# Kernel tuning notes

Hardware: AMD Instinct MI355X
Metric: run time of the kernel (lower is better)

Reference implementation:

```python
import jax, jax.numpy as jnp
import numpy as np

B, T, D = 8, 16384, 128


def setup_inputs() -> dict:
    key = jax.random.key(0)
    ks = jax.random.split(key, 14)
    sc = lambda fan_in: 1.0 / np.sqrt(fan_in)
    x = jax.random.normal(ks[0], (B, T, D), jnp.float32)
    return {
        "x": x,
        # BindingField (scale 0): bind_key / bind_query Linear(D, D//2)
        "Wk": jax.random.normal(ks[1], (D, D // 2), jnp.float32) * sc(D),
        "bk": jnp.zeros((D // 2,), jnp.float32),
        "Wq": jax.random.normal(ks[2], (D, D // 2), jnp.float32) * sc(D),
        "bq": jnp.zeros((D // 2,), jnp.float32),
        # aggregator (scale 0): Linear(D,D) -> LayerNorm(D) -> ReLU -> Linear(D,D)
        "Wa1": jax.random.normal(ks[3], (D, D), jnp.float32) * sc(D),
        "ba1": jnp.zeros((D,), jnp.float32),
        "ln_g": jnp.ones((D,), jnp.float32),
        "ln_b": jnp.zeros((D,), jnp.float32),
        "Wa2": jax.random.normal(ks[4], (D, D), jnp.float32) * sc(D),
        "ba2": jnp.zeros((D,), jnp.float32),
        # downward_influence (scale 0): Linear(D,D)
        "Wd": jax.random.normal(ks[5], (D, D), jnp.float32) * sc(D),
        "bd": jnp.zeros((D,), jnp.float32),
    }


def reference(x, Wk, bk, Wq, bq, Wa1, ba1, ln_g, ln_b, Wa2, ba2, Wd, bd):
    Bn, Tn, Dn = x.shape
    BIND_THRESHOLD = 0.5
    LN_EPS = 1e-5

    # ---- BindingField: binding strength between adjacent tokens ----
    keys = x[:, :-1] @ Wk + bk                       # [B, T-1, D/2]
    queries = x[:, 1:] @ Wq + bq                     # [B, T-1, D/2]
    strength = jax.nn.sigmoid((keys * queries).sum(-1) / float(np.sqrt(Dn // 2)))
    bind = strength > BIND_THRESHOLD                 # [B, T-1]

    # chunk_starts: token 0 always starts; token t starts iff NOT bound to t-1
    chunk_starts = jnp.concatenate([jnp.ones((Bn, 1), bool), ~bind], axis=1)
    seg = jnp.cumsum(chunk_starts.astype(jnp.int32), axis=1) - 1  # [B, T] chunk id per token

    # ---- aggregate_chunks: ragged mean-pool via segment_sum (pad to T chunk slots) ----
    seg_flat = (seg + jnp.arange(Bn, dtype=jnp.int32)[:, None] * Tn).reshape(-1)
    sums = jax.ops.segment_sum(x.reshape(-1, Dn), seg_flat, num_segments=Bn * Tn)
    counts = jax.ops.segment_sum(jnp.ones((Bn * Tn,), x.dtype), seg_flat,
                                 num_segments=Bn * Tn)
    chunk_mean = (sums / jnp.maximum(counts, 1.0)[:, None]).reshape(Bn, Tn, Dn)

    # aggregator MLP: Linear -> LayerNorm -> ReLU -> Linear
    h = chunk_mean @ Wa1 + ba1
    mu = h.mean(-1, keepdims=True)
    var = ((h - mu) ** 2).mean(-1, keepdims=True)    # biased var, as torch LayerNorm
    h = (h - mu) * jax.lax.rsqrt(var + LN_EPS) * ln_g + ln_b
    agg = jax.nn.relu(h) @ Wa2 + ba2                 # [B, T(chunk slots), D]

    # ---- apply_downward_influence: broadcast chunk signal back to its tokens ----
    infl = agg @ Wd + bd                             # [B, T(chunks), D]
    gathered = jnp.take_along_axis(infl, seg[..., None].astype(jnp.int32), axis=1)
    gate = jax.nn.sigmoid(gathered)
    return x * gate + x
```

## Files before the change

### kernel.cpp

```cpp
#include <hip/hip_runtime.h>
#include <math.h>

#define BB 8
#define TT 16384
#define DD 128
#define DH 64
#define FCAP 32768
#define FMARGIN 0.05f

typedef _Float16 half8 __attribute__((ext_vector_type(8)));
typedef float f32x4 __attribute__((ext_vector_type(4)));

union H8 { half8 h; uint4 q; ushort us[8]; };

static __device__ __forceinline__ float4 ld4(const float* p) { return *(const float4*)p; }

static __device__ __forceinline__ uint pk2(float a, float b) {
    union { _Float16 f; ushort u; } A, B;
    A.f = (_Float16)a; B.f = (_Float16)b;
    return (uint)A.u | ((uint)B.u << 16);
}

static __device__ __forceinline__ void split8h(const float4 v0, const float4 v1,
                                               half8* xh, half8* xl)
{
    float f[8] = {v0.x, v0.y, v0.z, v0.w, v1.x, v1.y, v1.z, v1.w};
    half8 h, l;
    #pragma unroll
    for (int j = 0; j < 8; ++j) {
        _Float16 hv = (_Float16)f[j];
        h[j] = hv;
        l[j] = (_Float16)(f[j] - (float)hv);
    }
    *xh = h; *xl = l;
}

__global__ __launch_bounds__(64) void k_wprep(
    const float* __restrict__ Wa1, const float* __restrict__ Wa2,
    const float* __restrict__ Wd, const float* __restrict__ Wk,
    const float* __restrict__ Wq, ushort* __restrict__ wfm,
    ushort* __restrict__ wfb, int* __restrict__ fcnt)
{
    const int l  = threadIdx.x;
    const int nt = blockIdx.x & 7;
    const int kb = blockIdx.x >> 3;
    const int ly = blockIdx.y;
    if (ly == 0 && blockIdx.x == 0 && l == 0) *fcnt = 0;
    const int n  = nt * 16 + (l & 15);
    const int k0 = kb * 32 + (l >> 4) * 8;
    H8 v;
    if (ly < 3) {
        const float* W = (ly == 0) ? Wa1 : (ly == 1) ? Wa2 : Wd;
        #pragma unroll
        for (int e = 0; e < 8; ++e) v.h[e] = (_Float16)W[(k0 + e) * DD + n];
        *(uint4*)(wfm + (size_t)(((ly * 8 + nt) * 4 + kb) * 64 + l) * 8) = v.q;
    } else {
        #pragma unroll
        for (int e = 0; e < 8; ++e) {
            float w = (n < 64) ? Wk[(k0 + e) * DH + n] : Wq[(k0 + e) * DH + n - 64];
            v.h[e] = (_Float16)w;
        }
        *(uint4*)(wfb + (size_t)((nt * 4 + kb) * 64 + l) * 8) = v.q;
    }
}

__global__ __launch_bounds__(256, 2) void k_bind(
    const float* __restrict__ x, const ushort* __restrict__ wfb,
    const float* __restrict__ bk, const float* __restrict__ bq,
    int* __restrict__ cstart, int* __restrict__ flist, int* __restrict__ fcnt)
{
    __shared__ uint4 Bs4[2048];
    __shared__ float bnd[4][64];
    const int b    = blockIdx.y;
    const int tb   = blockIdx.x * 64;
    const int tid  = threadIdx.x;
    const int wv   = tid >> 6;
    const int l    = tid & 63;
    const int lo16 = l & 15;
    const int g    = l >> 4;

    {
        const uint4* wsrc = (const uint4*)wfb;
        #pragma unroll
        for (int j = 0; j < 8; ++j) { int idx = tid + j * 256; Bs4[idx] = wsrc[idx]; }
    }

    const float* xrow = x + ((size_t)b * TT + tb + wv * 16 + lo16) * DD;
    half8 xh[4], xl[4];
    #pragma unroll
    for (int kb = 0; kb < 4; ++kb) {
        float4 v0 = ld4(xrow + kb * 32 + g * 8);
        float4 v1 = ld4(xrow + kb * 32 + g * 8 + 4);
        split8h(v0, v1, &xh[kb], &xl[kb]);
    }
    int r64 = tb + 64; if (r64 > TT - 1) r64 = TT - 1;
    const float* xq = x + ((size_t)b * TT + r64) * DD;
    half8 qh[4], ql[4];
    H8 z; z.q.x = z.q.y = z.q.z = z.q.w = 0u;
    #pragma unroll
    for (int kb = 0; kb < 4; ++kb) {
        qh[kb] = z.h; ql[kb] = z.h;
        if (lo16 == 0) {
            float4 v0 = ld4(xq + kb * 32 + g * 8);
            float4 v1 = ld4(xq + kb * 32 + g * 8 + 4);
            split8h(v0, v1, &qh[kb], &ql[kb]);
        }
    }

    f32x4 acc[8];
    #pragma unroll
    for (int nt = 0; nt < 8; ++nt) {
        int col = nt * 16 + lo16;
        float bias = (col < 64) ? bk[col] : bq[col - 64];
        acc[nt] = (f32x4){bias, bias, bias, bias};
    }
    f32x4 acc4;
    {
        float bias = bq[wv * 16 + lo16];
        acc4 = (f32x4){bias, bias, bias, bias};
    }

    __syncthreads();
    const ushort* Bs = (const ushort*)Bs4;
    const ushort* Bs_halo = Bs + (size_t)((4 + wv) * 4 * 64 + l) * 8;
    #pragma unroll
    for (int kb = 0; kb < 4; ++kb) {
        half8 bh[8];
        #pragma unroll
        for (int nt = 0; nt < 8; ++nt)
            bh[nt] = *(const half8*)(Bs + (size_t)((nt * 4 + kb) * 64 + l) * 8);
        #pragma unroll
        for (int nt = 0; nt < 8; ++nt) {
            acc[nt] = __builtin_amdgcn_mfma_f32_16x16x32_f16(xh[kb], bh[nt], acc[nt], 0, 0, 0);
            acc[nt] = __builtin_amdgcn_mfma_f32_16x16x32_f16(xl[kb], bh[nt], acc[nt], 0, 0, 0);
        }
        half8 bh4 = *(const half8*)(Bs_halo + (size_t)kb * 64 * 8);
        acc4 = __builtin_amdgcn_mfma_f32_16x16x32_f16(qh[kb], bh4, acc4, 0, 0, 0);
        acc4 = __builtin_amdgcn_mfma_f32_16x16x32_f16(ql[kb], bh4, acc4, 0, 0, 0);
    }

    if (l < 16) {
        if (wv > 0) {
            #pragma unroll
            for (int nt = 0; nt < 4; ++nt) bnd[wv - 1][nt * 16 + lo16] = acc[4 + nt][0];
        }
        bnd[3][wv * 16 + lo16] = acc4[0];
    }
    __syncthreads();

    float qn3[4];
    #pragma unroll
    for (int nt = 0; nt < 4; ++nt) qn3[nt] = __shfl_down(acc[4 + nt][0], 16);
    if (g == 3) {
        #pragma unroll
        for (int nt = 0; nt < 4; ++nt) qn3[nt] = bnd[wv][nt * 16 + lo16];
    }
    float s[4];
    #pragma unroll
    for (int i = 0; i < 3; ++i) {
        float t = 0.f;
        #pragma unroll
        for (int nt = 0; nt < 4; ++nt) t += acc[nt][i] * acc[4 + nt][i + 1];
        s[i] = t;
    }
    {
        float t = 0.f;
        #pragma unroll
        for (int nt = 0; nt < 4; ++nt) t += acc[nt][3] * qn3[nt];
        s[3] = t;
    }
    #pragma unroll
    for (int i = 0; i < 4; ++i) {
        #pragma unroll
        for (int m = 1; m < 16; m <<= 1) s[i] += __shfl_xor(s[i], m);
    }
    if (lo16 == 0) {
        #pragma unroll
        for (int i = 0; i < 4; ++i) {
            int t = tb + wv * 16 + g * 4 + i;
            if (t <= TT - 2) {
                cstart[b * TT + t + 1] = (s[i] > 0.f) ? 0 : 1;
                if (fabsf(s[i]) < FMARGIN) {
                    int pos = atomicAdd(fcnt, 1);
                    if (pos < FCAP) flist[pos] = b * TT + t;
                }
            }
        }
    }
    if (blockIdx.x == 0 && tid == 0) cstart[b * TT] = 1;
}

__global__ __launch_bounds__(256) void k_fixup(
    const float* __restrict__ x, const float* __restrict__ Wk, const float* __restrict__ bk,
    const float* __restrict__ Wq, const float* __restrict__ bq,
    const int* __restrict__ flist, const int* __restrict__ fcnt, int* __restrict__ cstart)
{
    const int n    = min(*fcnt, FCAP);
    const int wv   = (blockIdx.x * 256 + threadIdx.x) >> 6;
    const int lane = threadIdx.x & 63;
    const int nwv  = gridDim.x * 4;
    for (int i = wv; i < n; i += nwv) {
        int idx = flist[i];
        int b = idx >> 14;
        int t = idx & (TT - 1);
        const float* xt = x + ((size_t)b * TT + t) * DD;
        float K = bk[lane], Q = bq[lane];
        #pragma unroll 8
        for (int k = 0; k < DD; ++k) {
            K = fmaf(xt[k],      Wk[k * DH + lane], K);
            Q = fmaf(xt[DD + k], Wq[k * DH + lane], Q);
        }
        float p = K * Q;
        #pragma unroll
        for (int m = 1; m < 64; m <<= 1) p += __shfl_xor(p, m);
        if (lane == 0) cstart[b * TT + t + 1] = (p > 0.f) ? 0 : 1;
    }
}

__global__ __launch_bounds__(1024) void k_scan(const int* __restrict__ cstart,
    int* __restrict__ seg, int* __restrict__ cs, int* __restrict__ numC)
{
    __shared__ int wsum[16];
    const int b = blockIdx.x, tid = threadIdx.x;
    const int wv = tid >> 6, lane = tid & 63;
    const int base = b * TT + tid * 16;
    int v[16];
    #pragma unroll
    for (int i = 0; i < 4; ++i) {
        int4 q = *(const int4*)(cstart + base + i * 4);
        v[i * 4 + 0] = q.x; v[i * 4 + 1] = q.y; v[i * 4 + 2] = q.z; v[i * 4 + 3] = q.w;
    }
    int s[16]; int run = 0;
    #pragma unroll
    for (int i = 0; i < 16; ++i) { run += v[i]; s[i] = run; }
    int incl = run;
    #pragma unroll
    for (int off = 1; off < 64; off <<= 1) {
        int t = __shfl_up(incl, off);
        if (lane >= off) incl += t;
    }
    if (lane == 63) wsum[wv] = incl;
    __syncthreads();
    if (tid < 16) {
        int w = wsum[tid];
        #pragma unroll
        for (int off = 1; off < 16; off <<= 1) {
            int t = __shfl_up(w, off, 16);
            if (tid >= off) w += t;
        }
        wsum[tid] = w;
    }
    __syncthreads();
    const int excl = (wv ? wsum[wv - 1] : 0) + incl - run;
    #pragma unroll
    for (int i = 0; i < 16; ++i) {
        int sg = excl + s[i] - 1;
        seg[base + i] = sg;
        if (v[i]) cs[b * (TT + 1) + sg] = tid * 16 + i;
    }
    if (tid == 1023) {
        int tot = excl + run;
        numC[b] = tot;
        cs[b * (TT + 1) + tot] = TT;
    }
}

__device__ __forceinline__ void mlp_gemm(f32x4 acc[8], const uint4* Afr4,
    const ushort* Bs, int wv, int l)
{
    half8 af[4];
    #pragma unroll
    for (int kb = 0; kb < 4; ++kb)
        af[kb] = *(const half8*)((const char*)Afr4 + ((wv * 4 + kb) * 64 + l) * 16);
    #pragma unroll
    for (int kb = 0; kb < 4; ++kb) {
        half8 bh[8];
        #pragma unroll
        for (int nt = 0; nt < 8; ++nt)
            bh[nt] = *(const half8*)(Bs + (size_t)((nt * 4 + kb) * 64 + l) * 8);
        #pragma unroll
        for (int nt = 0; nt < 8; ++nt)
            acc[nt] = __builtin_amdgcn_mfma_f32_16x16x32_f16(af[kb], bh[nt], acc[nt], 0, 0, 0);
    }
}

__global__ __launch_bounds__(256, 2) void k_mlp(
    const float* __restrict__ x, const int* __restrict__ cs,
    const float* __restrict__ ba1, const float* __restrict__ ln_g, const float* __restrict__ ln_b,
    const float* __restrict__ ba2, const float* __restrict__ bd,
    const ushort* __restrict__ wfm, const int* __restrict__ numC, float* __restrict__ cm)
{
    __shared__ union {
        float Tok[64 * 132];
        struct { uint4 Afr[1024]; uint4 Bs[2048]; } fb;
    } sm;
    const int b  = blockIdx.y;
    const int nC = numC[b];
    const int c0 = blockIdx.x * 64;
    if (c0 >= nC) return;
    const int tid  = threadIdx.x;
    const int wv   = tid >> 6;
    const int l    = tid & 63;
    const int lo16 = l & 15;
    const int g    = l >> 4;
    const ushort* Bs = (const ushort*)sm.fb.Bs;
    const uint4* wsrc = (const uint4*)wfm;

    const int cbase = b * (TT + 1);
    const int T0 = cs[cbase + c0];
    const int cEnd = (c0 + 64 < nC) ? (c0 + 64) : nC;
    const int T1 = cs[cbase + cEnd];
    int t0r[8], t1r[8];
    #pragma unroll
    for (int ii = 0; ii < 8; ++ii) {
        int r = (tid + ii * 256) >> 5;
        int c = c0 + r;
        t0r[ii] = (c < nC) ? cs[cbase + c] : 0;
        t1r[ii] = (c < nC) ? cs[cbase + c + 1] : 0;
    }
    float4 vals[8];
    #pragma unroll
    for (int ii = 0; ii < 8; ++ii) vals[ii] = make_float4(0.f, 0.f, 0.f, 0.f);

    for (int tt = T0; tt < T1; tt += 64) {
        __syncthreads();
        const int tEnd = (tt + 64 < T1) ? (tt + 64) : T1;
        for (int j = tid; j < (tEnd - tt) * 32; j += 256) {
            int trow = j >> 5, c4 = (j & 31) * 4;
            *(float4*)&sm.Tok[trow * 132 + c4] =
                ld4(x + ((size_t)b * TT + tt + trow) * DD + c4);
        }
        __syncthreads();
        #pragma unroll
        for (int ii = 0; ii < 8; ++ii) {
            int c4 = ((tid + ii * 256) & 31) * 4;
            int lo = (t0r[ii] > tt)   ? t0r[ii] : tt;
            int hi = (t1r[ii] < tEnd) ? t1r[ii] : tEnd;
            for (int t = lo; t < hi; ++t) {
                const float* ap = &sm.Tok[(t - tt) * 132 + c4];
                vals[ii].x += ap[0]; vals[ii].y += ap[1];
                vals[ii].z += ap[2]; vals[ii].w += ap[3];
            }
        }
    }
    __syncthreads();

    #pragma unroll
    for (int ii = 0; ii < 8; ++ii) {
        int i = tid + ii * 256;
        int r = i >> 5, c4 = (i & 31) * 4;
        float4 sv = make_float4(0.f, 0.f, 0.f, 0.f);
        if (c0 + r < nC) {
            float inv = 1.f / (float)(t1r[ii] - t0r[ii]);
            sv.x = vals[ii].x * inv; sv.y = vals[ii].y * inv;
            sv.z = vals[ii].z * inv; sv.w = vals[ii].w * inv;
        }
        int frag = (r >> 4) * 4 + (c4 >> 5);
        int lanef = (r & 15) + (((c4 & 31) >> 3) * 16);
        uint2 pk = make_uint2(pk2(sv.x, sv.y), pk2(sv.z, sv.w));
        *(uint2*)((char*)sm.fb.Afr + frag * 1024 + lanef * 16 + (c4 & 7) * 2) = pk;
    }
    #pragma unroll
    for (int j = 0; j < 8; ++j) { int idx = tid + j * 256; sm.fb.Bs[idx] = wsrc[idx]; }
    __syncthreads();

    f32x4 acc[8];
    #pragma unroll
    for (int nt = 0; nt < 8; ++nt) {
        float bias = ba1[nt * 16 + lo16];
        acc[nt] = (f32x4){bias, bias, bias, bias};
    }
    mlp_gemm(acc, sm.fb.Afr, Bs, wv, l);

    float mu_[4], rs_[4];
    #pragma unroll
    for (int i = 0; i < 4; ++i) {
        float smv = 0.f;
        #pragma unroll
        for (int nt = 0; nt < 8; ++nt) smv += acc[nt][i];
        #pragma unroll
        for (int k = 1; k < 16; k <<= 1) smv += __shfl_xor(smv, k, 16);
        mu_[i] = smv * (1.f / 128.f);
        float vs = 0.f;
        #pragma unroll
        for (int nt = 0; nt < 8; ++nt) { float d = acc[nt][i] - mu_[i]; vs += d * d; }
        #pragma unroll
        for (int k = 1; k < 16; k <<= 1) vs += __shfl_xor(vs, k, 16);
        rs_[i] = rsqrtf(vs * (1.f / 128.f) + 1e-5f);
    }
    float gam[8], bet[8];
    #pragma unroll
    for (int nt = 0; nt < 8; ++nt) { gam[nt] = ln_g[nt * 16 + lo16]; bet[nt] = ln_b[nt * 16 + lo16]; }

    __syncthreads();
    #pragma unroll
    for (int nt = 0; nt < 8; ++nt) {
        int cw = nt * 16 + lo16;
        int frag = wv * 4 + (cw >> 5);
        int lnf  = (((cw & 31) >> 3) * 16);
        #pragma unroll
        for (int i = 0; i < 4; ++i) {
            float h = fmaf((acc[nt][i] - mu_[i]) * rs_[i], gam[nt], bet[nt]);
            union { _Float16 f; ushort u; } cv; cv.f = (_Float16)fmaxf(h, 0.f);
            *((ushort*)((char*)sm.fb.Afr + frag * 1024 + ((g * 4 + i) + lnf) * 16 + (cw & 7) * 2)) = cv.u;
        }
    }
    #pragma unroll
    for (int j = 0; j < 8; ++j) { int idx = tid + j * 256; sm.fb.Bs[idx] = wsrc[2048 + idx]; }
    __syncthreads();

    #pragma unroll
    for (int nt = 0; nt < 8; ++nt) {
        float bias = ba2[nt * 16 + lo16];
        acc[nt] = (f32x4){bias, bias, bias, bias};
    }
    mlp_gemm(acc, sm.fb.Afr, Bs, wv, l);
    __syncthreads();
    #pragma unroll
    for (int nt = 0; nt < 8; ++nt) {
        int cw = nt * 16 + lo16;
        int frag = wv * 4 + (cw >> 5);
        int lnf  = (((cw & 31) >> 3) * 16);
        #pragma unroll
        for (int i = 0; i < 4; ++i) {
            union { _Float16 f; ushort u; } cv; cv.f = (_Float16)acc[nt][i];
            *((ushort*)((char*)sm.fb.Afr + frag * 1024 + ((g * 4 + i) + lnf) * 16 + (cw & 7) * 2)) = cv.u;
        }
    }
    #pragma unroll
    for (int j = 0; j < 8; ++j) { int idx = tid + j * 256; sm.fb.Bs[idx] = wsrc[4096 + idx]; }
    __syncthreads();

    #pragma unroll
    for (int nt = 0; nt < 8; ++nt) {
        float bias = bd[nt * 16 + lo16];
        acc[nt] = (f32x4){bias, bias, bias, bias};
    }
    mlp_gemm(acc, sm.fb.Afr, Bs, wv, l);
    #pragma unroll
    for (int i = 0; i < 4; ++i) {
        int row = c0 + wv * 16 + g * 4 + i;
        if (row < nC) {
            float* dst = cm + ((size_t)b * TT + row) * DD + lo16;
            #pragma unroll
            for (int nt = 0; nt < 8; ++nt)
                dst[nt * 16] = 1.f / (1.f + __expf(-acc[nt][i]));
        }
    }
}

__global__ __launch_bounds__(256) void k_out(const float* __restrict__ x,
    const int* __restrict__ seg, const float* __restrict__ gate, float* __restrict__ out)
{
    const size_t idx = (size_t)blockIdx.x * 256 + threadIdx.x;
    const size_t tok = idx >> 5;
    const int d4 = (int)(idx & 31);
    const int b  = (int)(tok >> 14);
    const int sg = seg[tok];
    float4 gv = ld4(gate + (((size_t)b << 14) + sg) * DD + d4 * 4);
    float4 xv = ld4(x + tok * DD + (size_t)d4 * 4);
    float4 o;
    o.x = fmaf(xv.x, gv.x, xv.x);
    o.y = fmaf(xv.y, gv.y, xv.y);
    o.z = fmaf(xv.z, gv.z, xv.z);
    o.w = fmaf(xv.w, gv.w, xv.w);
    *(float4*)(out + idx * 4) = o;
}

extern "C" void kernel_launch(void* const* d_in, const int* in_sizes, int n_in,
                              void* d_out, int out_size, void* d_ws, size_t ws_size,
                              hipStream_t stream)
{
    (void)in_sizes; (void)n_in; (void)out_size; (void)ws_size;
    const float* x    = (const float*)d_in[0];
    const float* Wk   = (const float*)d_in[1];
    const float* bk   = (const float*)d_in[2];
    const float* Wq   = (const float*)d_in[3];
    const float* bq   = (const float*)d_in[4];
    const float* Wa1  = (const float*)d_in[5];
    const float* ba1  = (const float*)d_in[6];
    const float* ln_g = (const float*)d_in[7];
    const float* ln_b = (const float*)d_in[8];
    const float* Wa2  = (const float*)d_in[9];
    const float* ba2  = (const float*)d_in[10];
    const float* Wd   = (const float*)d_in[11];
    const float* bd   = (const float*)d_in[12];
    float* out = (float*)d_out;

    char* p = (char*)d_ws;
    float* cm    = (float*)p;   p += (size_t)BB * TT * DD * 4;
    int* seg     = (int*)p;     p += (size_t)BB * TT * 4;
    int* cs      = (int*)p;     p += (size_t)BB * (TT + 1) * 4;
    int* numC    = (int*)p;     p += 64;
    ushort* wfm  = (ushort*)p;  p += 3 * DD * DD * 2;
    ushort* wfb  = (ushort*)p;  p += DD * DD * 2;
    int* flist   = (int*)p;     p += (size_t)FCAP * 4;
    int* fcnt    = (int*)p;

    k_wprep<<<dim3(32, 4), 64, 0, stream>>>(Wa1, Wa2, Wd, Wk, Wq, wfm, wfb, fcnt);
    k_bind<<<dim3(256, BB), 256, 0, stream>>>(x, wfb, bk, bq, seg, flist, fcnt);
    k_fixup<<<dim3(256), 256, 0, stream>>>(x, Wk, bk, Wq, bq, flist, fcnt, seg);
    k_scan<<<dim3(BB), 1024, 0, stream>>>(seg, seg, cs, numC);
    k_mlp<<<dim3(TT / 64, BB), 256, 0, stream>>>(x, cs, ba1, ln_g, ln_b, ba2, bd, wfm, numC, cm);
    k_out<<<dim3(BB * TT * DD / (256 * 4)), 256, 0, stream>>>(x, seg, cm, out);
}
```

Measured before the change: 118.2 us.

## Fuse gated output into MLP kernel and prefetch weights through registers

Removes the separate output kernel and the chunk-gate buffer in global memory. Each MLP block now stages its 64 sigmoid gates (plus one) in shared memory and writes the outputs for all tokens its chunks cover, re-reading x for that token range. Weight tiles for the next GEMM are also prefetched into registers before the preceding shared-memory phase, which hides global load latency but adds register pressure at the 2-blocks-per-SM bound. Saves the gate write and read plus one kernel launch, but the output pass is now serialized inside each block after the three GEMMs.

```diff
diff --git a/kernel.cpp b/kernel.cpp
--- a/kernel.cpp
+++ b/kernel.cpp
@@ -285,10 +285,10 @@
 }
 
 __global__ __launch_bounds__(256, 2) void k_mlp(
-    const float* __restrict__ x, const int* __restrict__ cs,
+    const float* __restrict__ x, const int* __restrict__ cs, const int* __restrict__ seg,
     const float* __restrict__ ba1, const float* __restrict__ ln_g, const float* __restrict__ ln_b,
     const float* __restrict__ ba2, const float* __restrict__ bd,
-    const ushort* __restrict__ wfm, const int* __restrict__ numC, float* __restrict__ cm)
+    const ushort* __restrict__ wfm, const int* __restrict__ numC, float* __restrict__ out)
 {
     __shared__ union {
         float Tok[64 * 132];
@@ -306,6 +306,10 @@
     const ushort* Bs = (const ushort*)sm.fb.Bs;
     const uint4* wsrc = (const uint4*)wfm;
 
+    uint4 breg[8];
+    #pragma unroll
+    for (int j = 0; j < 8; ++j) breg[j] = wsrc[tid + j * 256];
+
     const int cbase = b * (TT + 1);
     const int T0 = cs[cbase + c0];
     const int cEnd = (c0 + 64 < nC) ? (c0 + 64) : nC;
@@ -346,6 +350,8 @@
     __syncthreads();
 
     #pragma unroll
+    for (int j = 0; j < 8; ++j) sm.fb.Bs[tid + j * 256] = breg[j];
+    #pragma unroll
     for (int ii = 0; ii < 8; ++ii) {
         int i = tid + ii * 256;
         int r = i >> 5, c4 = (i & 31) * 4;
@@ -361,7 +367,7 @@
         *(uint2*)((char*)sm.fb.Afr + frag * 1024 + lanef * 16 + (c4 & 7) * 2) = pk;
     }
     #pragma unroll
-    for (int j = 0; j < 8; ++j) { int idx = tid + j * 256; sm.fb.Bs[idx] = wsrc[idx]; }
+    for (int j = 0; j < 8; ++j) breg[j] = wsrc[2048 + tid + j * 256];
     __syncthreads();
 
     f32x4 acc[8];
@@ -406,7 +412,9 @@
         }
     }
     #pragma unroll
-    for (int j = 0; j < 8; ++j) { int idx = tid + j * 256; sm.fb.Bs[idx] = wsrc[2048 + idx]; }
+    for (int j = 0; j < 8; ++j) sm.fb.Bs[tid + j * 256] = breg[j];
+    #pragma unroll
+    for (int j = 0; j < 8; ++j) breg[j] = wsrc[4096 + tid + j * 256];
     __syncthreads();
 
     #pragma unroll
@@ -428,7 +436,7 @@
         }
     }
     #pragma unroll
-    for (int j = 0; j < 8; ++j) { int idx = tid + j * 256; sm.fb.Bs[idx] = wsrc[4096 + idx]; }
+    for (int j = 0; j < 8; ++j) sm.fb.Bs[tid + j * 256] = breg[j];
     __syncthreads();
 
     #pragma unroll
@@ -437,34 +445,29 @@
         acc[nt] = (f32x4){bias, bias, bias, bias};
     }
     mlp_gemm(acc, sm.fb.Afr, Bs, wv, l);
-    #pragma unroll
-    for (int i = 0; i < 4; ++i) {
-        int row = c0 + wv * 16 + g * 4 + i;
-        if (row < nC) {
-            float* dst = cm + ((size_t)b * TT + row) * DD + lo16;
-            #pragma unroll
-            for (int nt = 0; nt < 8; ++nt)
-                dst[nt * 16] = 1.f / (1.f + __expf(-acc[nt][i]));
-        }
-    }
-}
-
-__global__ __launch_bounds__(256) void k_out(const float* __restrict__ x,
-    const int* __restrict__ seg, const float* __restrict__ gate, float* __restrict__ out)
-{
-    const size_t idx = (size_t)blockIdx.x * 256 + threadIdx.x;
-    const size_t tok = idx >> 5;
-    const int d4 = (int)(idx & 31);
-    const int b  = (int)(tok >> 14);
-    const int sg = seg[tok];
-    float4 gv = ld4(gate + (((size_t)b << 14) + sg) * DD + d4 * 4);
-    float4 xv = ld4(x + tok * DD + (size_t)d4 * 4);
-    float4 o;
-    o.x = fmaf(xv.x, gv.x, xv.x);
-    o.y = fmaf(xv.y, gv.y, xv.y);
-    o.z = fmaf(xv.z, gv.z, xv.z);
-    o.w = fmaf(xv.w, gv.w, xv.w);
-    *(float4*)(out + idx * 4) = o;
+    __syncthreads();
+
+    #pragma unroll
+    for (int nt = 0; nt < 8; ++nt) {
+        #pragma unroll
+        for (int i = 0; i < 4; ++i) {
+            int row = wv * 16 + g * 4 + i;
+            sm.Tok[row * 132 + nt * 16 + lo16] = 1.f + 1.f / (1.f + __expf(-acc[nt][i]));
+        }
+    }
+    __syncthreads();
+
+    for (int j = tid; j < (T1 - T0) * 32; j += 256) {
+        int tok = T0 + (j >> 5);
+        int c4  = (j & 31) * 4;
+        int row = seg[b * TT + tok] - c0;
+        float4 xv = ld4(x + ((size_t)b * TT + tok) * DD + c4);
+        float4 gv = *(const float4*)&sm.Tok[row * 132 + c4];
+        float4 o;
+        o.x = xv.x * gv.x; o.y = xv.y * gv.y;
+        o.z = xv.z * gv.z; o.w = xv.w * gv.w;
+        *(float4*)(out + ((size_t)b * TT + tok) * DD + c4) = o;
+    }
 }
 
 extern "C" void kernel_launch(void* const* d_in, const int* in_sizes, int n_in,
@@ -488,7 +491,7 @@
     float* out = (float*)d_out;
 
     char* p = (char*)d_ws;
-    float* cm    = (float*)p;   p += (size_t)BB * TT * DD * 4;
+    p += (size_t)BB * TT * DD * 4;
     int* seg     = (int*)p;     p += (size_t)BB * TT * 4;
     int* cs      = (int*)p;     p += (size_t)BB * (TT + 1) * 4;
     int* numC    = (int*)p;     p += 64;
@@ -501,6 +504,5 @@
     k_bind<<<dim3(256, BB), 256, 0, stream>>>(x, wfb, bk, bq, seg, flist, fcnt);
     k_fixup<<<dim3(256), 256, 0, stream>>>(x, Wk, bk, Wq, bq, flist, fcnt, seg);
     k_scan<<<dim3(BB), 1024, 0, stream>>>(seg, seg, cs, numC);
-    k_mlp<<<dim3(TT / 64, BB), 256, 0, stream>>>(x, cs, ba1, ln_g, ln_b, ba2, bd, wfm, numC, cm);
-    k_out<<<dim3(BB * TT * DD / (256 * 4)), 256, 0, stream>>>(x, seg, cm, out);
-}
+    k_mlp<<<dim3(TT / 64, BB), 256, 0, stream>>>(x, cs, seg, ba1, ln_g, ln_b, ba2, bd, wfm, numC, out);
+}
```

After: 129.9 us. 1.1x slower.

## Halve MLP chunk tile, prefetch weights in registers, store gate as fp16

Applied to the files above, without the earlier changes.

The chunk-MLP kernel now handles 32 chunks per block instead of 64, so twice as many blocks share the ragged workload and only two of the four waves run the GEMMs. Weight fragments for the next layer are prefetched into registers while the current stage computes, which hides the global load latency behind the pooling and GEMM work. The gate tensor is written and read as fp16 instead of fp32, halving gate traffic between the MLP and output kernels. The cost is idle waves during the GEMMs and a small precision loss in the gate.

```diff
diff --git a/kernel.cpp b/kernel.cpp
--- a/kernel.cpp
+++ b/kernel.cpp
@@ -19,6 +19,12 @@
     union { _Float16 f; ushort u; } A, B;
     A.f = (_Float16)a; B.f = (_Float16)b;
     return (uint)A.u | ((uint)B.u << 16);
+}
+static __device__ __forceinline__ ushort f2h(float a) {
+    union { _Float16 f; ushort u; } A; A.f = (_Float16)a; return A.u;
+}
+static __device__ __forceinline__ float h2f(ushort u) {
+    union { ushort u; _Float16 f; } A; A.u = u; return (float)A.f;
 }
 
 static __device__ __forceinline__ void split8h(const float4 v0, const float4 v1,
@@ -288,15 +294,15 @@
     const float* __restrict__ x, const int* __restrict__ cs,
     const float* __restrict__ ba1, const float* __restrict__ ln_g, const float* __restrict__ ln_b,
     const float* __restrict__ ba2, const float* __restrict__ bd,
-    const ushort* __restrict__ wfm, const int* __restrict__ numC, float* __restrict__ cm)
+    const ushort* __restrict__ wfm, const int* __restrict__ numC, ushort* __restrict__ gate2)
 {
     __shared__ union {
         float Tok[64 * 132];
-        struct { uint4 Afr[1024]; uint4 Bs[2048]; } fb;
+        struct { uint4 Afr[512]; uint4 Bs[2048]; } fb;
     } sm;
     const int b  = blockIdx.y;
     const int nC = numC[b];
-    const int c0 = blockIdx.x * 64;
+    const int c0 = blockIdx.x * 32;
     if (c0 >= nC) return;
     const int tid  = threadIdx.x;
     const int wv   = tid >> 6;
@@ -306,21 +312,25 @@
     const ushort* Bs = (const ushort*)sm.fb.Bs;
     const uint4* wsrc = (const uint4*)wfm;
 
+    uint4 breg[8];
+    #pragma unroll
+    for (int j = 0; j < 8; ++j) breg[j] = wsrc[tid + j * 256];
+
     const int cbase = b * (TT + 1);
     const int T0 = cs[cbase + c0];
-    const int cEnd = (c0 + 64 < nC) ? (c0 + 64) : nC;
+    const int cEnd = (c0 + 32 < nC) ? (c0 + 32) : nC;
     const int T1 = cs[cbase + cEnd];
-    int t0r[8], t1r[8];
-    #pragma unroll
-    for (int ii = 0; ii < 8; ++ii) {
+    int t0r[4], t1r[4];
+    #pragma unroll
+    for (int ii = 0; ii < 4; ++ii) {
         int r = (tid + ii * 256) >> 5;
         int c = c0 + r;
         t0r[ii] = (c < nC) ? cs[cbase + c] : 0;
         t1r[ii] = (c < nC) ? cs[cbase + c + 1] : 0;
     }
-    float4 vals[8];
-    #pragma unroll
-    for (int ii = 0; ii < 8; ++ii) vals[ii] = make_float4(0.f, 0.f, 0.f, 0.f);
+    float4 vals[4];
+    #pragma unroll
+    for (int ii = 0; ii < 4; ++ii) vals[ii] = make_float4(0.f, 0.f, 0.f, 0.f);
 
     for (int tt = T0; tt < T1; tt += 64) {
         __syncthreads();
@@ -332,7 +342,7 @@
         }
         __syncthreads();
         #pragma unroll
-        for (int ii = 0; ii < 8; ++ii) {
+        for (int ii = 0; ii < 4; ++ii) {
             int c4 = ((tid + ii * 256) & 31) * 4;
             int lo = (t0r[ii] > tt)   ? t0r[ii] : tt;
             int hi = (t1r[ii] < tEnd) ? t1r[ii] : tEnd;
@@ -346,7 +356,9 @@
     __syncthreads();
 
     #pragma unroll
-    for (int ii = 0; ii < 8; ++ii) {
+    for (int j = 0; j < 8; ++j) sm.fb.Bs[tid + j * 256] = breg[j];
+    #pragma unroll
+    for (int ii = 0; ii < 4; ++ii) {
         int i = tid + ii * 256;
         int r = i >> 5, c4 = (i & 31) * 4;
         float4 sv = make_float4(0.f, 0.f, 0.f, 0.f);
@@ -361,109 +373,115 @@
         *(uint2*)((char*)sm.fb.Afr + frag * 1024 + lanef * 16 + (c4 & 7) * 2) = pk;
     }
     #pragma unroll
-    for (int j = 0; j < 8; ++j) { int idx = tid + j * 256; sm.fb.Bs[idx] = wsrc[idx]; }
+    for (int j = 0; j < 8; ++j) breg[j] = wsrc[2048 + tid + j * 256];
     __syncthreads();
 
     f32x4 acc[8];
-    #pragma unroll
-    for (int nt = 0; nt < 8; ++nt) {
-        float bias = ba1[nt * 16 + lo16];
-        acc[nt] = (f32x4){bias, bias, bias, bias};
-    }
-    mlp_gemm(acc, sm.fb.Afr, Bs, wv, l);
-
-    float mu_[4], rs_[4];
-    #pragma unroll
-    for (int i = 0; i < 4; ++i) {
-        float smv = 0.f;
-        #pragma unroll
-        for (int nt = 0; nt < 8; ++nt) smv += acc[nt][i];
-        #pragma unroll
-        for (int k = 1; k < 16; k <<= 1) smv += __shfl_xor(smv, k, 16);
-        mu_[i] = smv * (1.f / 128.f);
-        float vs = 0.f;
-        #pragma unroll
-        for (int nt = 0; nt < 8; ++nt) { float d = acc[nt][i] - mu_[i]; vs += d * d; }
-        #pragma unroll
-        for (int k = 1; k < 16; k <<= 1) vs += __shfl_xor(vs, k, 16);
-        rs_[i] = rsqrtf(vs * (1.f / 128.f) + 1e-5f);
-    }
-    float gam[8], bet[8];
-    #pragma unroll
-    for (int nt = 0; nt < 8; ++nt) { gam[nt] = ln_g[nt * 16 + lo16]; bet[nt] = ln_b[nt * 16 + lo16]; }
-
-    __syncthreads();
-    #pragma unroll
-    for (int nt = 0; nt < 8; ++nt) {
-        int cw = nt * 16 + lo16;
-        int frag = wv * 4 + (cw >> 5);
-        int lnf  = (((cw & 31) >> 3) * 16);
+    float mu_[4], rs_[4], gam[8], bet[8];
+    if (wv < 2) {
+        #pragma unroll
+        for (int nt = 0; nt < 8; ++nt) {
+            float bias = ba1[nt * 16 + lo16];
+            acc[nt] = (f32x4){bias, bias, bias, bias};
+        }
+        mlp_gemm(acc, sm.fb.Afr, Bs, wv, l);
         #pragma unroll
         for (int i = 0; i < 4; ++i) {
-            float h = fmaf((acc[nt][i] - mu_[i]) * rs_[i], gam[nt], bet[nt]);
-            union { _Float16 f; ushort u; } cv; cv.f = (_Float16)fmaxf(h, 0.f);
-            *((ushort*)((char*)sm.fb.Afr + frag * 1024 + ((g * 4 + i) + lnf) * 16 + (cw & 7) * 2)) = cv.u;
-        }
-    }
-    #pragma unroll
-    for (int j = 0; j < 8; ++j) { int idx = tid + j * 256; sm.fb.Bs[idx] = wsrc[2048 + idx]; }
-    __syncthreads();
-
-    #pragma unroll
-    for (int nt = 0; nt < 8; ++nt) {
-        float bias = ba2[nt * 16 + lo16];
-        acc[nt] = (f32x4){bias, bias, bias, bias};
-    }
-    mlp_gemm(acc, sm.fb.Afr, Bs, wv, l);
-    __syncthreads();
-    #pragma unroll
-    for (int nt = 0; nt < 8; ++nt) {
-        int cw = nt * 16 + lo16;
-        int frag = wv * 4 + (cw >> 5);
-        int lnf  = (((cw & 31) >> 3) * 16);
+            float smv = 0.f;
+            #pragma unroll
+            for (int nt = 0; nt < 8; ++nt) smv += acc[nt][i];
+            #pragma unroll
+            for (int k = 1; k < 16; k <<= 1) smv += __shfl_xor(smv, k, 16);
+            mu_[i] = smv * (1.f / 128.f);
+            float vs = 0.f;
+            #pragma unroll
+            for (int nt = 0; nt < 8; ++nt) { float d = acc[nt][i] - mu_[i]; vs += d * d; }
+            #pragma unroll
+            for (int k = 1; k < 16; k <<= 1) vs += __shfl_xor(vs, k, 16);
+            rs_[i] = rsqrtf(vs * (1.f / 128.f) + 1e-5f);
+        }
+        #pragma unroll
+        for (int nt = 0; nt < 8; ++nt) { gam[nt] = ln_g[nt * 16 + lo16]; bet[nt] = ln_b[nt * 16 + lo16]; }
+    }
+    __syncthreads();
+    if (wv < 2) {
+        #pragma unroll
+        for (int nt = 0; nt < 8; ++nt) {
+            int cw = nt * 16 + lo16;
+            int frag = wv * 4 + (cw >> 5);
+            int lnf  = (((cw & 31) >> 3) * 16);
+            #pragma unroll
+            for (int i = 0; i < 4; ++i) {
+                float h = fmaf((acc[nt][i] - mu_[i]) * rs_[i], gam[nt], bet[nt]);
+                *((ushort*)((char*)sm.fb.Afr + frag * 1024 + ((g * 4 + i) + lnf) * 16 + (cw & 7) * 2)) = f2h(fmaxf(h, 0.f));
+            }
+        }
+    }
+    #pragma unroll
+    for (int j = 0; j < 8; ++j) sm.fb.Bs[tid + j * 256] = breg[j];
+    #pragma unroll
+    for (int j = 0; j < 8; ++j) breg[j] = wsrc[4096 + tid + j * 256];
+    __syncthreads();
+
+    if (wv < 2) {
+        #pragma unroll
+        for (int nt = 0; nt < 8; ++nt) {
+            float bias = ba2[nt * 16 + lo16];
+            acc[nt] = (f32x4){bias, bias, bias, bias};
+        }
+        mlp_gemm(acc, sm.fb.Afr, Bs, wv, l);
+    }
+    __syncthreads();
+    if (wv < 2) {
+        #pragma unroll
+        for (int nt = 0; nt < 8; ++nt) {
+            int cw = nt * 16 + lo16;
+            int frag = wv * 4 + (cw >> 5);
+            int lnf  = (((cw & 31) >> 3) * 16);
+            #pragma unroll
+            for (int i = 0; i < 4; ++i)
+                *((ushort*)((char*)sm.fb.Afr + frag * 1024 + ((g * 4 + i) + lnf) * 16 + (cw & 7) * 2)) = f2h(acc[nt][i]);
+        }
+    }
+    #pragma unroll
+    for (int j = 0; j < 8; ++j) sm.fb.Bs[tid + j * 256] = breg[j];
+    __syncthreads();
+
+    if (wv < 2) {
+        #pragma unroll
+        for (int nt = 0; nt < 8; ++nt) {
+            float bias = bd[nt * 16 + lo16];
+            acc[nt] = (f32x4){bias, bias, bias, bias};
+        }
+        mlp_gemm(acc, sm.fb.Afr, Bs, wv, l);
         #pragma unroll
         for (int i = 0; i < 4; ++i) {
-            union { _Float16 f; ushort u; } cv; cv.f = (_Float16)acc[nt][i];
-            *((ushort*)((char*)sm.fb.Afr + frag * 1024 + ((g * 4 + i) + lnf) * 16 + (cw & 7) * 2)) = cv.u;
-        }
-    }
-    #pragma unroll
-    for (int j = 0; j < 8; ++j) { int idx = tid + j * 256; sm.fb.Bs[idx] = wsrc[4096 + idx]; }
-    __syncthreads();
-
-    #pragma unroll
-    for (int nt = 0; nt < 8; ++nt) {
-        float bias = bd[nt * 16 + lo16];
-        acc[nt] = (f32x4){bias, bias, bias, bias};
-    }
-    mlp_gemm(acc, sm.fb.Afr, Bs, wv, l);
-    #pragma unroll
-    for (int i = 0; i < 4; ++i) {
-        int row = c0 + wv * 16 + g * 4 + i;
-        if (row < nC) {
-            float* dst = cm + ((size_t)b * TT + row) * DD + lo16;
-            #pragma unroll
-            for (int nt = 0; nt < 8; ++nt)
-                dst[nt * 16] = 1.f / (1.f + __expf(-acc[nt][i]));
+            int row = c0 + wv * 16 + g * 4 + i;
+            if (row < nC) {
+                ushort* dst = gate2 + ((size_t)b * TT + row) * DD + lo16;
+                #pragma unroll
+                for (int nt = 0; nt < 8; ++nt)
+                    dst[nt * 16] = f2h(1.f / (1.f + __expf(-acc[nt][i])));
+            }
         }
     }
 }
 
 __global__ __launch_bounds__(256) void k_out(const float* __restrict__ x,
-    const int* __restrict__ seg, const float* __restrict__ gate, float* __restrict__ out)
+    const int* __restrict__ seg, const ushort* __restrict__ gate2, float* __restrict__ out)
 {
     const size_t idx = (size_t)blockIdx.x * 256 + threadIdx.x;
     const size_t tok = idx >> 5;
     const int d4 = (int)(idx & 31);
     const int b  = (int)(tok >> 14);
     const int sg = seg[tok];
-    float4 gv = ld4(gate + (((size_t)b << 14) + sg) * DD + d4 * 4);
+    ushort4 gu = *(const ushort4*)(gate2 + (((size_t)b << 14) + sg) * DD + d4 * 4);
     float4 xv = ld4(x + tok * DD + (size_t)d4 * 4);
     float4 o;
-    o.x = fmaf(xv.x, gv.x, xv.x);
-    o.y = fmaf(xv.y, gv.y, xv.y);
-    o.z = fmaf(xv.z, gv.z, xv.z);
-    o.w = fmaf(xv.w, gv.w, xv.w);
+    o.x = fmaf(xv.x, h2f(gu.x), xv.x);
+    o.y = fmaf(xv.y, h2f(gu.y), xv.y);
+    o.z = fmaf(xv.z, h2f(gu.z), xv.z);
+    o.w = fmaf(xv.w, h2f(gu.w), xv.w);
     *(float4*)(out + idx * 4) = o;
 }
 
@@ -488,7 +506,7 @@
     float* out = (float*)d_out;
 
     char* p = (char*)d_ws;
-    float* cm    = (float*)p;   p += (size_t)BB * TT * DD * 4;
+    ushort* gate2 = (ushort*)p; p += (size_t)BB * TT * DD * 4;
     int* seg     = (int*)p;     p += (size_t)BB * TT * 4;
     int* cs      = (int*)p;     p += (size_t)BB * (TT + 1) * 4;
     int* numC    = (int*)p;     p += 64;
@@ -501,6 +519,6 @@
     k_bind<<<dim3(256, BB), 256, 0, stream>>>(x, wfb, bk, bq, seg, flist, fcnt);
     k_fixup<<<dim3(256), 256, 0, stream>>>(x, Wk, bk, Wq, bq, flist, fcnt, seg);
     k_scan<<<dim3(BB), 1024, 0, stream>>>(seg, seg, cs, numC);
-    k_mlp<<<dim3(TT / 64, BB), 256, 0, stream>>>(x, cs, ba1, ln_g, ln_b, ba2, bd, wfm, numC, cm);
-    k_out<<<dim3(BB * TT * DD / (256 * 4)), 256, 0, stream>>>(x, seg, cm, out);
-}
+    k_mlp<<<dim3(TT / 32, BB), 256, 0, stream>>>(x, cs, ba1, ln_g, ln_b, ba2, bd, wfm, numC, gate2);
+    k_out<<<dim3(BB * TT * DD / (256 * 4)), 256, 0, stream>>>(x, seg, gate2, out);
+}
```

After: 154.9 us. +31.0%, slower.

## Double-buffer token tiles and prefetch MLP weights through registers in k_mlp

Applied to the files above, without the earlier changes.

The segment-sum stage now stages token rows in two 32-row LDS buffers. Global loads for the next tile are issued into registers before the current tile is accumulated, then written to the other buffer afterward, which removes one barrier per iteration and hides load latency. The weight matrices for each of the three GEMMs are likewise prefetched into registers one stage ahead, so global latency overlaps prior compute. In exchange, the tile is smaller (more iterations) and the extra register arrays (breg, ldv) raise register pressure under launch_bounds(256,2).

```diff
diff --git a/kernel.cpp b/kernel.cpp
--- a/kernel.cpp
+++ b/kernel.cpp
@@ -291,7 +291,7 @@
     const ushort* __restrict__ wfm, const int* __restrict__ numC, float* __restrict__ cm)
 {
     __shared__ union {
-        float Tok[64 * 132];
+        float Tok[2][32 * 132];
         struct { uint4 Afr[1024]; uint4 Bs[2048]; } fb;
     } sm;
     const int b  = blockIdx.y;
@@ -306,6 +306,10 @@
     const ushort* Bs = (const ushort*)sm.fb.Bs;
     const uint4* wsrc = (const uint4*)wfm;
 
+    uint4 breg[8];
+    #pragma unroll
+    for (int j = 0; j < 8; ++j) breg[j] = wsrc[tid + j * 256];
+
     const int cbase = b * (TT + 1);
     const int T0 = cs[cbase + c0];
     const int cEnd = (c0 + 64 < nC) ? (c0 + 64) : nC;
@@ -322,29 +326,52 @@
     #pragma unroll
     for (int ii = 0; ii < 8; ++ii) vals[ii] = make_float4(0.f, 0.f, 0.f, 0.f);
 
-    for (int tt = T0; tt < T1; tt += 64) {
+    {
+        int tEnd0 = (T0 + 32 < T1) ? (T0 + 32) : T1;
+        for (int j = tid; j < (tEnd0 - T0) * 32; j += 256) {
+            int trow = j >> 5, c4 = (j & 31) * 4;
+            *(float4*)&sm.Tok[0][trow * 132 + c4] =
+                ld4(x + ((size_t)b * TT + T0 + trow) * DD + c4);
+        }
+    }
+    int buf = 0;
+    for (int tt = T0; tt < T1; tt += 32) {
         __syncthreads();
-        const int tEnd = (tt + 64 < T1) ? (tt + 64) : T1;
-        for (int j = tid; j < (tEnd - tt) * 32; j += 256) {
-            int trow = j >> 5, c4 = (j & 31) * 4;
-            *(float4*)&sm.Tok[trow * 132 + c4] =
-                ld4(x + ((size_t)b * TT + tt + trow) * DD + c4);
-        }
-        __syncthreads();
+        const int tEnd = (tt + 32 < T1) ? (tt + 32) : T1;
+        float4 ldv[4]; int ldst[4];
+        const int nEnd = (tt + 64 < T1) ? (tt + 64) : T1;
+        const int nwords = (tt + 32 < T1) ? (nEnd - (tt + 32)) * 32 : 0;
+        #pragma unroll
+        for (int k2 = 0; k2 < 4; ++k2) {
+            int j = tid + k2 * 256;
+            ldst[k2] = -1;
+            ldv[k2] = make_float4(0.f, 0.f, 0.f, 0.f);
+            if (j < nwords) {
+                int trow = j >> 5, c4 = (j & 31) * 4;
+                ldv[k2] = ld4(x + ((size_t)b * TT + tt + 32 + trow) * DD + c4);
+                ldst[k2] = trow * 132 + c4;
+            }
+        }
         #pragma unroll
         for (int ii = 0; ii < 8; ++ii) {
             int c4 = ((tid + ii * 256) & 31) * 4;
             int lo = (t0r[ii] > tt)   ? t0r[ii] : tt;
             int hi = (t1r[ii] < tEnd) ? t1r[ii] : tEnd;
             for (int t = lo; t < hi; ++t) {
-                const float* ap = &sm.Tok[(t - tt) * 132 + c4];
+                const float* ap = &sm.Tok[buf][(t - tt) * 132 + c4];
                 vals[ii].x += ap[0]; vals[ii].y += ap[1];
                 vals[ii].z += ap[2]; vals[ii].w += ap[3];
             }
         }
-    }
-    __syncthreads();
-
+        #pragma unroll
+        for (int k2 = 0; k2 < 4; ++k2)
+            if (ldst[k2] >= 0) *(float4*)&sm.Tok[buf ^ 1][ldst[k2]] = ldv[k2];
+        buf ^= 1;
+    }
+    __syncthreads();
+
+    #pragma unroll
+    for (int j = 0; j < 8; ++j) sm.fb.Bs[tid + j * 256] = breg[j];
     #pragma unroll
     for (int ii = 0; ii < 8; ++ii) {
         int i = tid + ii * 256;
@@ -361,7 +388,7 @@
         *(uint2*)((char*)sm.fb.Afr + frag * 1024 + lanef * 16 + (c4 & 7) * 2) = pk;
     }
     #pragma unroll
-    for (int j = 0; j < 8; ++j) { int idx = tid + j * 256; sm.fb.Bs[idx] = wsrc[idx]; }
+    for (int j = 0; j < 8; ++j) breg[j] = wsrc[2048 + tid + j * 256];
     __syncthreads();
 
     f32x4 acc[8];
@@ -406,7 +433,9 @@
         }
     }
     #pragma unroll
-    for (int j = 0; j < 8; ++j) { int idx = tid + j * 256; sm.fb.Bs[idx] = wsrc[2048 + idx]; }
+    for (int j = 0; j < 8; ++j) sm.fb.Bs[tid + j * 256] = breg[j];
+    #pragma unroll
+    for (int j = 0; j < 8; ++j) breg[j] = wsrc[4096 + tid + j * 256];
     __syncthreads();
 
     #pragma unroll
@@ -428,7 +457,7 @@
         }
     }
     #pragma unroll
-    for (int j = 0; j < 8; ++j) { int idx = tid + j * 256; sm.fb.Bs[idx] = wsrc[4096 + idx]; }
+    for (int j = 0; j < 8; ++j) sm.fb.Bs[tid + j * 256] = breg[j];
     __syncthreads();
 
     #pragma unroll
```

After: 138.3 us. 17.0% more time.
